# Kernel optimization log

Hardware: AMD Instinct MI355X
Metric: run time of the kernel (lower is better)

## Reference

```python
import jax, jax.numpy as jnp
import numpy as np

B, N, C, W = 256, 4096, 16, 10
L = N - W + 1
EPS = 1e-5


def setup_inputs() -> dict:
    key = jax.random.key(0)
    ks = jax.random.split(key, 6)
    def lin(k, shape, fan_in):
        # mimic nn.Linear default init scale ~ U(-1/sqrt(fan), 1/sqrt(fan))
        b = 1.0 / np.sqrt(fan_in)
        return jax.random.uniform(k, shape, jnp.float32, -b, b)
    return {
        "x": jax.random.normal(ks[0], (B, N, C, 2), jnp.float32),
        "W_in_real": lin(ks[1], (C, L), L),      # per-channel input filter (real)
        "W_in_imag": lin(ks[2], (C, L), L),      # per-channel input filter (imag)
        "W_nl": lin(ks[3], (C, 2, 2 * C), 2 * C),  # per-channel Linear(2C -> 2)
        "W_out_real": lin(ks[4], (C, W), W),      # per-channel output filter (real)
        "W_out_imag": lin(ks[5], (C, W), W),      # per-channel output filter (imag)
        "gamma": jnp.ones((C,), jnp.float32),     # BatchNorm1d weight
        "beta": jnp.zeros((C,), jnp.float32),     # BatchNorm1d bias
    }


def _depthwise_valid(x_bcn, w_cl):
    # sliding dot-products f[:, c, id] = sum_l x[:, c, id+l] * w[c, l]
    # == depthwise 1D valid correlation: [B,C,N] * [C,L] -> [B,C,W]
    nC = w_cl.shape[0]
    return jax.lax.conv_general_dilated(
        x_bcn, w_cl[:, None, :], window_strides=(1,), padding='VALID',
        dimension_numbers=('NCH', 'OIH', 'NCH'), feature_group_count=nC)


def reference(x, W_in_real, W_in_imag, W_nl, W_out_real, W_out_imag, gamma, beta):
    xr = jnp.transpose(x[..., 0], (0, 2, 1))  # [B,C,N]
    xi = jnp.transpose(x[..., 1], (0, 2, 1))
    # stage 1: per-channel windowed filters + amplitude (|f|^2) scaling
    fr = jnp.transpose(_depthwise_valid(xr, W_in_real), (0, 2, 1))  # [B,W,C]
    fi = jnp.transpose(_depthwise_valid(xi, W_in_imag), (0, 2, 1))  # [B,W,C]
    amp = fr * fr + fi * fi
    fr = amp * fr
    fi = amp * fi
    # stage 2: per-channel nonlin Linear(2C -> 2) on cat([real, imag])
    tf = jnp.concatenate([fr, fi], axis=-1)            # [B,W,2C]
    nl = jnp.einsum('bwi,coi->bwco', tf, W_nl)         # [B,W,C,2]
    nr, ni = nl[..., 0], nl[..., 1]                    # [B,W,C]
    # stage 3: per-channel output filters over the out_window dim
    out_r = jnp.einsum('bwc,cw->bc', nr, W_out_real)   # [B,C]
    out_i = jnp.einsum('bwc,cw->bc', ni, W_out_imag)   # [B,C]
    out = jnp.stack([out_r, out_i], axis=-1)           # [B,C,2]
    # BatchNorm1d(n_channels) in training mode: stats over (batch, last) per channel
    mean = out.mean(axis=(0, 2), keepdims=True)
    var = out.var(axis=(0, 2), keepdims=True)
    return (out - mean) / jnp.sqrt(var + EPS) * gamma[None, :, None] + beta[None, :, None]
```

## Files before the change

kernel.cpp:

```cpp
#include <hip/hip_runtime.h>

#define BB 256
#define NN 4096
#define CC 16
#define WW 10
#define LL 4087
#define EPSF 1e-5f

#define GLOAD16(gsrc, ldst)                                                                  \
    __builtin_amdgcn_global_load_lds((const __attribute__((address_space(1))) void*)(gsrc),  \
                                     (__attribute__((address_space(3))) void*)(ldst), 16, 0, 0)

__global__ __launch_bounds__(256) void pack_weights(const float* __restrict__ Wr,
                                                    const float* __restrict__ Wi,
                                                    float2* __restrict__ pk) {
    int tg = blockIdx.x * 256 + threadIdx.x;
    int n = tg >> 4, c = tg & 15;
    float2 v = make_float2(0.f, 0.f);
    if (n < LL) { v.x = Wr[c * LL + n]; v.y = Wi[c * LL + n]; }
    pk[tg] = v;
}

__global__ __launch_bounds__(1024, 4) void fused_lds(const float* __restrict__ x,
                                                     const float2* __restrict__ pk,
                                                     const float* __restrict__ Wnl,
                                                     const float* __restrict__ Wor,
                                                     const float* __restrict__ Woi,
                                                     float* __restrict__ outraw) {
    __shared__ __align__(16) char smem[135168];

    const int b = blockIdx.x;
    const int tid = threadIdx.x;
    const int c = tid & 15;
    const int tc = tid >> 4;
    const int base = tc * 4;
    const int lane = tid & 63, wave = tid >> 6;
    const int l16 = lane * 16;

    const char* __restrict__ xsrc = (const char*)x + (size_t)b * (NN * CC * 8);
    const char* __restrict__ psrc = (const char*)pk;

    float fr[WW], fi[WW];
#pragma unroll
    for (int w = 0; w < WW; ++w) { fr[w] = 0.f; fi[w] = 0.f; }

    {
#pragma unroll
        for (int k = 0; k < 2; ++k) {
            const int i = wave * 2 + k;
            GLOAD16(xsrc + i * 1024 + l16, smem + i * 1024);
            GLOAD16(psrc + i * 1024 + l16, smem + 65536 + i * 1024);
        }
        if (wave < 2) {
            const int i = 32 + wave;
            GLOAD16(psrc + i * 1024 + l16, smem + 65536 + i * 1024);
        }
    }
    __syncthreads();

#pragma unroll 1
    for (int t = 0; t < 16; ++t) {
        if (t < 15) {
            const int t1 = t + 1, pb_ = t1 & 1;
            const char* xs = xsrc + (size_t)t1 * 32768;
            char* xd = smem + pb_ * 32768;
#pragma unroll
            for (int k = 0; k < 2; ++k) {
                const int i = wave * 2 + k;
                GLOAD16(xs + i * 1024 + l16, xd + i * 1024);
            }
            const char* ps = psrc + (size_t)(t1 * 256 - 16) * 128;
            char* pd = smem + 65536 + pb_ * 34816;
#pragma unroll
            for (int k = 0; k < 2; ++k) {
                const int i = wave * 2 + k;
                GLOAD16(ps + i * 1024 + l16, pd + i * 1024);
            }
            if (wave < 2) {
                const int i = 32 + wave;
                GLOAD16(ps + i * 1024 + l16, pd + i * 1024);
            }
        }

        const float2* __restrict__ xb = (const float2*)(smem + (t & 1) * 32768);
        const float2* __restrict__ pb = (const float2*)(smem + 65536 + (t & 1) * 34816);

        float2 wv[13];
        if (t == 0) {
#pragma unroll
            for (int k = 0; k < 13; ++k) {
                const int slot = base + k - 9;
                const int sc = slot < 0 ? 0 : slot;
                const float2 tmp = pb[sc * 16 + c];
                wv[k].x = (slot >= 0) ? tmp.x : 0.f;
                wv[k].y = (slot >= 0) ? tmp.y : 0.f;
            }
        } else {
#pragma unroll
            for (int k = 0; k < 13; ++k) wv[k] = pb[(base + 7 + k) * 16 + c];
        }
        float2 xv[4];
#pragma unroll
        for (int j = 0; j < 4; ++j) xv[j] = xb[(base + j) * 16 + c];
#pragma unroll
        for (int j = 0; j < 4; ++j) {
#pragma unroll
            for (int w = 0; w < WW; ++w) {
                const int k = j - w + 9;
                fr[w] += xv[j].x * wv[k].x;
                fi[w] += xv[j].y * wv[k].y;
            }
        }
        __syncthreads();
    }

#pragma unroll
    for (int w = 0; w < WW; ++w) {
        fr[w] += __shfl_xor(fr[w], 16);
        fr[w] += __shfl_xor(fr[w], 32);
        fi[w] += __shfl_xor(fi[w], 16);
        fi[w] += __shfl_xor(fi[w], 32);
    }
    float (*red)[320] = (float (*)[320])smem;
    float* F2 = (float*)(smem + 20480);
    float* nls = (float*)(smem + 21760);
    if (lane < 16) {
#pragma unroll
        for (int w = 0; w < WW; ++w) {
            red[wave][lane * 20 + w] = fr[w];
            red[wave][lane * 20 + 10 + w] = fi[w];
        }
    }
    __syncthreads();
    if (tid < 320) {
        float s = 0.f;
#pragma unroll
        for (int k = 0; k < 16; ++k) s += red[k][tid];
        F2[tid] = s;
    }
    __syncthreads();
    if (tid < 160) {
        const int cc = tid / 10, w = tid % 10;
        const float a = F2[cc * 20 + w], q = F2[cc * 20 + 10 + w];
        const float amp = a * a + q * q;
        F2[cc * 20 + w] = a * amp;
        F2[cc * 20 + 10 + w] = q * amp;
    }
    __syncthreads();
    if (tid < 320) {
        const int cc = tid / 20, rem = tid % 20, o = rem / 10, w = rem % 10;
        const float* __restrict__ wn = Wnl + (cc * 2 + o) * 32;
        float acc = 0.f;
#pragma unroll
        for (int i = 0; i < 16; ++i) acc += F2[i * 20 + w] * wn[i];
#pragma unroll
        for (int i = 0; i < 16; ++i) acc += F2[i * 20 + 10 + w] * wn[16 + i];
        nls[tid] = acc;
    }
    __syncthreads();
    if (tid < 32) {
        const int cc = tid >> 1, o = tid & 1;
        const float* __restrict__ wo = (o == 0 ? Wor : Woi) + cc * WW;
        float acc = 0.f;
#pragma unroll
        for (int w = 0; w < WW; ++w) acc += nls[cc * 20 + o * 10 + w] * wo[w];
        outraw[b * 32 + cc * 2 + o] = acc;
    }
}

__global__ __launch_bounds__(1024, 4) void fused_main_nopk(const float* __restrict__ x,
                                                           const float* __restrict__ Wr,
                                                           const float* __restrict__ Wi,
                                                           const float* __restrict__ Wnl,
                                                           const float* __restrict__ Wor,
                                                           const float* __restrict__ Woi,
                                                           float* __restrict__ outraw) {
    const int b = blockIdx.x;
    const int tid = threadIdx.x;
    const int tc = tid >> 4;
    const int c = tid & 15;
    const int n0 = tc * 64;

    const float2* __restrict__ x2 = (const float2*)x + (size_t)b * (NN * CC) + (n0 * 16 + c);

    float tr[9], ti[9];
    float fr[WW], fi[WW];
#pragma unroll
    for (int w = 0; w < WW; ++w) { fr[w] = 0.f; fi[w] = 0.f; }

#pragma unroll
    for (int j = 0; j < 9; ++j) {
        const int m = n0 - 9 + j;
        const int mc = m < 0 ? 0 : m;
        const float a = Wr[c * LL + mc], q = Wi[c * LL + mc];
        tr[j] = (m >= 0) ? a : 0.f;
        ti[j] = (m >= 0) ? q : 0.f;
    }

#pragma unroll 1
    for (int g = 0; g < 4; ++g) {
        const int nb = n0 + g * 16;
        float2 xb[16], wb[16];
#pragma unroll
        for (int p = 0; p < 16; ++p) {
            xb[p] = x2[p * 16];
            const int n = nb + p;
            const int nc2 = (n < LL) ? n : (LL - 1);
            const float a = Wr[c * LL + nc2], q = Wi[c * LL + nc2];
            wb[p].x = (n < LL) ? a : 0.f;
            wb[p].y = (n < LL) ? q : 0.f;
        }
        x2 += 256;
#pragma unroll
        for (int p = 0; p < 16; ++p) {
#pragma unroll
            for (int w = 0; w < WW; ++w) {
                const int q = p - w;
                const float wr_ = (q >= 0) ? wb[q].x : tr[q + 9];
                const float wi_ = (q >= 0) ? wb[q].y : ti[q + 9];
                fr[w] += xb[p].x * wr_;
                fi[w] += xb[p].y * wi_;
            }
        }
#pragma unroll
        for (int j = 0; j < 9; ++j) { tr[j] = wb[j + 7].x; ti[j] = wb[j + 7].y; }
    }

#pragma unroll
    for (int w = 0; w < WW; ++w) {
        fr[w] += __shfl_xor(fr[w], 16);
        fr[w] += __shfl_xor(fr[w], 32);
        fi[w] += __shfl_xor(fi[w], 16);
        fi[w] += __shfl_xor(fi[w], 32);
    }
    __shared__ float red[16][320];
    __shared__ float F2[320];
    __shared__ float nls[320];
    const int lane = tid & 63, wave = tid >> 6;
    if (lane < 16) {
#pragma unroll
        for (int w = 0; w < WW; ++w) {
            red[wave][lane * 20 + w] = fr[w];
            red[wave][lane * 20 + 10 + w] = fi[w];
        }
    }
    __syncthreads();
    if (tid < 320) {
        float s = 0.f;
#pragma unroll
        for (int k = 0; k < 16; ++k) s += red[k][tid];
        F2[tid] = s;
    }
    __syncthreads();
    if (tid < 160) {
        const int cc = tid / 10, w = tid % 10;
        const float a = F2[cc * 20 + w], q = F2[cc * 20 + 10 + w];
        const float amp = a * a + q * q;
        F2[cc * 20 + w] = a * amp;
        F2[cc * 20 + 10 + w] = q * amp;
    }
    __syncthreads();
    if (tid < 320) {
        const int cc = tid / 20, rem = tid % 20, o = rem / 10, w = rem % 10;
        const float* __restrict__ wn = Wnl + (cc * 2 + o) * 32;
        float acc = 0.f;
#pragma unroll
        for (int i = 0; i < 16; ++i) acc += F2[i * 20 + w] * wn[i];
#pragma unroll
        for (int i = 0; i < 16; ++i) acc += F2[i * 20 + 10 + w] * wn[16 + i];
        nls[tid] = acc;
    }
    __syncthreads();
    if (tid < 32) {
        const int cc = tid >> 1, o = tid & 1;
        const float* __restrict__ wo = (o == 0 ? Wor : Woi) + cc * WW;
        float acc = 0.f;
#pragma unroll
        for (int w = 0; w < WW; ++w) acc += nls[cc * 20 + o * 10 + w] * wo[w];
        outraw[b * 32 + cc * 2 + o] = acc;
    }
}

__global__ __launch_bounds__(256) void bnorm(float* __restrict__ out,
                                             const float* __restrict__ gamma,
                                             const float* __restrict__ beta) {
    const int c = blockIdx.x;
    const int t = threadIdx.x;
    const float v0 = out[t * 32 + c * 2 + 0];
    const float v1 = out[t * 32 + c * 2 + 1];
    float s = v0 + v1;
    float ss = v0 * v0 + v1 * v1;
#pragma unroll
    for (int off = 32; off > 0; off >>= 1) {
        s += __shfl_down(s, off, 64);
        ss += __shfl_down(ss, off, 64);
    }
    __shared__ float ls[8];
    const int wave = t >> 6, lane = t & 63;
    if (lane == 0) { ls[wave * 2] = s; ls[wave * 2 + 1] = ss; }
    __syncthreads();
    const float S = ls[0] + ls[2] + ls[4] + ls[6];
    const float SS = ls[1] + ls[3] + ls[5] + ls[7];
    const float mean = S * (1.f / 512.f);
    const float var = SS * (1.f / 512.f) - mean * mean;
    const float scale = gamma[c] * rsqrtf(var + EPSF);
    const float sh = beta[c];
    out[t * 32 + c * 2 + 0] = (v0 - mean) * scale + sh;
    out[t * 32 + c * 2 + 1] = (v1 - mean) * scale + sh;
}

extern "C" void kernel_launch(void* const* d_in, const int* in_sizes, int n_in,
                              void* d_out, int out_size, void* d_ws, size_t ws_size,
                              hipStream_t stream) {
    const float* x     = (const float*)d_in[0];
    const float* Wr    = (const float*)d_in[1];
    const float* Wi    = (const float*)d_in[2];
    const float* Wnl   = (const float*)d_in[3];
    const float* Wor   = (const float*)d_in[4];
    const float* Woi   = (const float*)d_in[5];
    const float* gamma = (const float*)d_in[6];
    const float* beta  = (const float*)d_in[7];
    float* out = (float*)d_out;

    const size_t pk_bytes = (size_t)NN * CC * sizeof(float2);
    float2* pk = (float2*)d_ws;
    const bool use_pk = (ws_size >= pk_bytes);

    if (use_pk) {
        hipLaunchKernelGGL(pack_weights, dim3(256), dim3(256), 0, stream, Wr, Wi, pk);
        hipLaunchKernelGGL(fused_lds, dim3(BB), dim3(1024), 0, stream,
                           x, pk, Wnl, Wor, Woi, out);
    } else {
        hipLaunchKernelGGL(fused_main_nopk, dim3(BB), dim3(1024), 0, stream,
                           x, Wr, Wi, Wnl, Wor, Woi, out);
    }
    hipLaunchKernelGGL(bnorm, dim3(CC), dim3(256), 0, stream, out, gamma, beta);
}
```

Baseline: 212.2 us.

## Replace double-buffered LDS staging with a four-slot ring pipeline and smaller tiles

Changes the main convolution loop from 16 double-buffered tiles to 32 smaller tiles held in a four-slot LDS ring, issued two stages ahead. Each wave now waits on its own load count with an explicit vmcnt wait plus a raw s_barrier, instead of a full __syncthreads per iteration. Window weights that straddle a tile boundary are read from the previous ring slot instead of loading an overlapping halo, which removes the extra 2KB of weight reload per tile and the 34816-byte padded buffers. The aim is to overlap global-to-LDS copies with the FMA work and to cut barrier stalls. In exchange it runs twice as many loop iterations, with less work per thread per iteration, and it depends on hand-written waitcnt ordering being correct.

```diff
diff --git a/kernel.cpp b/kernel.cpp
--- a/kernel.cpp
+++ b/kernel.cpp
@@ -21,98 +21,77 @@
     pk[tg] = v;
 }
 
-__global__ __launch_bounds__(1024, 4) void fused_lds(const float* __restrict__ x,
-                                                     const float2* __restrict__ pk,
-                                                     const float* __restrict__ Wnl,
-                                                     const float* __restrict__ Wor,
-                                                     const float* __restrict__ Woi,
-                                                     float* __restrict__ outraw) {
-    __shared__ __align__(16) char smem[135168];
+__global__ __launch_bounds__(1024, 4) void fused_pipe(const float* __restrict__ x,
+                                                      const float2* __restrict__ pk,
+                                                      const float* __restrict__ Wnl,
+                                                      const float* __restrict__ Wor,
+                                                      const float* __restrict__ Woi,
+                                                      float* __restrict__ outraw) {
+    __shared__ __align__(16) char smem[131072];
 
     const int b = blockIdx.x;
     const int tid = threadIdx.x;
     const int c = tid & 15;
     const int tc = tid >> 4;
-    const int base = tc * 4;
+    const int base = tc * 2;
     const int lane = tid & 63, wave = tid >> 6;
-    const int l16 = lane * 16;
-
-    const char* __restrict__ xsrc = (const char*)x + (size_t)b * (NN * CC * 8);
-    const char* __restrict__ psrc = (const char*)pk;
+
+    const char* __restrict__ xsrc =
+        (const char*)x + (size_t)b * (NN * CC * 8) + wave * 1024 + lane * 16;
+    const char* __restrict__ psrc = (const char*)pk + wave * 1024 + lane * 16;
+
+#define STAGE(u)                                                            \
+    do {                                                                    \
+        GLOAD16(xsrc + (size_t)(u) * 16384,                                 \
+                smem + ((u) & 3) * 16384 + wave * 1024);                    \
+        GLOAD16(psrc + (size_t)(u) * 16384,                                 \
+                smem + 65536 + ((u) & 3) * 16384 + wave * 1024);            \
+    } while (0)
 
     float fr[WW], fi[WW];
 #pragma unroll
     for (int w = 0; w < WW; ++w) { fr[w] = 0.f; fi[w] = 0.f; }
 
-    {
-#pragma unroll
-        for (int k = 0; k < 2; ++k) {
-            const int i = wave * 2 + k;
-            GLOAD16(xsrc + i * 1024 + l16, smem + i * 1024);
-            GLOAD16(psrc + i * 1024 + l16, smem + 65536 + i * 1024);
-        }
-        if (wave < 2) {
-            const int i = 32 + wave;
-            GLOAD16(psrc + i * 1024 + l16, smem + 65536 + i * 1024);
-        }
-    }
-    __syncthreads();
+    STAGE(0);
+    STAGE(1);
+    if (tid < 288) ((float*)(smem + 65536 + 3 * 16384 + 119 * 128))[tid] = 0.f;
+    asm volatile("s_waitcnt lgkmcnt(0)" ::: "memory");
 
 #pragma unroll 1
-    for (int t = 0; t < 16; ++t) {
-        if (t < 15) {
-            const int t1 = t + 1, pb_ = t1 & 1;
-            const char* xs = xsrc + (size_t)t1 * 32768;
-            char* xd = smem + pb_ * 32768;
-#pragma unroll
-            for (int k = 0; k < 2; ++k) {
-                const int i = wave * 2 + k;
-                GLOAD16(xs + i * 1024 + l16, xd + i * 1024);
-            }
-            const char* ps = psrc + (size_t)(t1 * 256 - 16) * 128;
-            char* pd = smem + 65536 + pb_ * 34816;
-#pragma unroll
-            for (int k = 0; k < 2; ++k) {
-                const int i = wave * 2 + k;
-                GLOAD16(ps + i * 1024 + l16, pd + i * 1024);
-            }
-            if (wave < 2) {
-                const int i = 32 + wave;
-                GLOAD16(ps + i * 1024 + l16, pd + i * 1024);
-            }
-        }
-
-        const float2* __restrict__ xb = (const float2*)(smem + (t & 1) * 32768);
-        const float2* __restrict__ pb = (const float2*)(smem + 65536 + (t & 1) * 34816);
-
-        float2 wv[13];
-        if (t == 0) {
-#pragma unroll
-            for (int k = 0; k < 13; ++k) {
-                const int slot = base + k - 9;
-                const int sc = slot < 0 ? 0 : slot;
-                const float2 tmp = pb[sc * 16 + c];
-                wv[k].x = (slot >= 0) ? tmp.x : 0.f;
-                wv[k].y = (slot >= 0) ? tmp.y : 0.f;
-            }
+    for (int t = 0; t < 32; ++t) {
+        if (t < 31) {
+            asm volatile("s_waitcnt vmcnt(2)" ::: "memory");
         } else {
-#pragma unroll
-            for (int k = 0; k < 13; ++k) wv[k] = pb[(base + 7 + k) * 16 + c];
-        }
-        float2 xv[4];
-#pragma unroll
-        for (int j = 0; j < 4; ++j) xv[j] = xb[(base + j) * 16 + c];
-#pragma unroll
-        for (int j = 0; j < 4; ++j) {
-#pragma unroll
-            for (int w = 0; w < WW; ++w) {
-                const int k = j - w + 9;
-                fr[w] += xv[j].x * wv[k].x;
-                fi[w] += xv[j].y * wv[k].y;
-            }
-        }
-        __syncthreads();
-    }
+            asm volatile("s_waitcnt vmcnt(0)" ::: "memory");
+        }
+        __builtin_amdgcn_s_barrier();
+        __builtin_amdgcn_sched_barrier(0);
+
+        if (t + 2 < 32) STAGE(t + 2);
+
+        const float2* __restrict__ xb = (const float2*)(smem + (t & 3) * 16384);
+        const float2* __restrict__ pc = (const float2*)(smem + 65536 + (t & 3) * 16384);
+        const float2* __restrict__ pp = (const float2*)(smem + 65536 + ((t + 3) & 3) * 16384);
+
+        float2 wv[11];
+#pragma unroll
+        for (int k = 0; k < 11; ++k) {
+            const int r = base + k - 9;
+            const float2* __restrict__ sp =
+                (r < 0) ? (pp + ((r + 128) * 16 + c)) : (pc + (r * 16 + c));
+            wv[k] = *sp;
+        }
+        const float2 xv0 = xb[base * 16 + c];
+        const float2 xv1 = xb[(base + 1) * 16 + c];
+#pragma unroll
+        for (int w = 0; w < WW; ++w) {
+            fr[w] += xv0.x * wv[9 - w].x;
+            fi[w] += xv0.y * wv[9 - w].y;
+            fr[w] += xv1.x * wv[10 - w].x;
+            fi[w] += xv1.y * wv[10 - w].y;
+        }
+    }
+#undef STAGE
 
 #pragma unroll
     for (int w = 0; w < WW; ++w) {
@@ -328,7 +307,7 @@
 
     if (use_pk) {
         hipLaunchKernelGGL(pack_weights, dim3(256), dim3(256), 0, stream, Wr, Wi, pk);
-        hipLaunchKernelGGL(fused_lds, dim3(BB), dim3(1024), 0, stream,
+        hipLaunchKernelGGL(fused_pipe, dim3(BB), dim3(1024), 0, stream,
                            x, pk, Wnl, Wor, Woi, out);
     } else {
         hipLaunchKernelGGL(fused_main_nopk, dim3(BB), dim3(1024), 0, stream,
```

Result: slower. 217.0 us (+2.2%).
